# Optimization experiments

Measured on AMD Instinct MI355X. Metric: run time of the kernel, lower is better.

The kernel has to match this reference:

```python
import jax, jax.numpy as jnp
import numpy as np

D_MODEL = 1024
N_HEADS = 16
D_H = D_MODEL // N_HEADS
MAX_LEN = 2048
BATCH = 2
SEQ = 2048
EPS = 1e-8
W_SCALE = 0.02


def _rms_norm(x, w):
    # RMSNorm: x * rsqrt(mean(x^2) + eps) * w
    ms = jnp.mean(jnp.square(x), axis=-1, keepdims=True)
    return w * (x * jax.lax.rsqrt(ms + EPS))


def setup_inputs() -> dict:
    key = jax.random.key(0)
    ks = jax.random.split(key, 12)
    d = D_MODEL
    inp = {
        "x": jax.random.normal(ks[0], (BATCH, SEQ, d), dtype=jnp.float32),
        "t_bias": jnp.zeros((1,), dtype=jnp.float32),  # unused by the module
        "p_bias": jax.random.normal(ks[1], (MAX_LEN, N_HEADS), dtype=jnp.float32),
        # AMS layer params (Linear stored as [in, out])
        "wq": jax.random.normal(ks[2], (d, d), dtype=jnp.float32) * W_SCALE,
        "bq": jnp.zeros((d,), dtype=jnp.float32),
        "wk": jax.random.normal(ks[3], (d, d), dtype=jnp.float32) * W_SCALE,
        "bk": jnp.zeros((d,), dtype=jnp.float32),
        "wv": jax.random.normal(ks[4], (d, d), dtype=jnp.float32) * W_SCALE,
        "bv": jnp.zeros((d,), dtype=jnp.float32),
        "wu": jax.random.normal(ks[5], (d, d), dtype=jnp.float32) * W_SCALE,
        "bu": jnp.zeros((d,), dtype=jnp.float32),
        "g_ams": jnp.ones((d,), dtype=jnp.float32),   # shared RMSNorm weight in AMSLayer
        # MFFN layer params
        "w0": jax.random.normal(ks[6], (d, d), dtype=jnp.float32) * W_SCALE,
        "b0": jnp.zeros((d,), dtype=jnp.float32),
        "w1": jax.random.normal(ks[7], (d, 2 * d), dtype=jnp.float32) * W_SCALE,
        "b1": jnp.zeros((2 * d,), dtype=jnp.float32),
        "w2": jax.random.normal(ks[8], (d, d), dtype=jnp.float32) * W_SCALE,
        "b2": jnp.zeros((d,), dtype=jnp.float32),
        "g_mffn": jnp.ones((d,), dtype=jnp.float32),
    }
    return inp


def reference(x, t_bias, p_bias, wq, bq, wk, bk, wv, bv, wu, bu, g_ams,
              w0, b0, w1, b1, w2, b2, g_mffn):
    B, S, d = x.shape
    H, dh = N_HEADS, D_H

    # ---- AMS layer ----
    x_norm = _rms_norm(x, g_ams)

    def proj(w, b):
        # [B,S,d] -> [B,H,S,dh]
        return (x_norm @ w + b).reshape(B, S, H, dh).transpose(0, 2, 1, 3)

    q = proj(wq, bq)
    k = proj(wk, bk)
    v = proj(wv, bv)

    scale = 1.0 / np.sqrt(dh).astype(np.float32)
    score = jnp.einsum('bhsd,bhtd->bhst', q, k) * scale
    # additive positional bias: p_bias[:S].T -> [H,S], broadcast over query dim
    score = score + p_bias[:S, :].T[None, :, None, :]

    attn = jax.nn.silu(score)                        # SiLU instead of softmax
    out = jnp.einsum('bhst,bhtd->bhsd', attn, v)
    out = out.transpose(0, 2, 1, 3).reshape(B, S, d)

    u = jax.nn.silu(x_norm @ wu + bu)
    ams_out = _rms_norm(out, g_ams) * u

    # ---- MFFN layer ----
    o = (ams_out @ w0 + b0) + x
    o_norm = _rms_norm(o, g_mffn)
    x12 = o_norm @ w1 + b1
    x1, x2 = jnp.split(x12, 2, axis=-1)
    swiglu = jax.nn.silu(x1) * x2
    return (swiglu @ w2 + b2) + o
```

## Files before the change

kernel.cpp:

```cpp
#include <hip/hip_runtime.h>
#include <stdint.h>
#include <math.h>


#define D    1024
#define NH   16
#define DH   64
#define B_   2
#define S_   2048
#define ROWS 4096
#define LQ   4096
#define EPSR 1e-8f

typedef unsigned short u16;
typedef __attribute__((ext_vector_type(8))) short short8;
typedef __attribute__((ext_vector_type(4))) float f32x4;

__device__ __forceinline__ float bf2f(u16 u) {
    union { uint32_t i; float f; } c; c.i = ((uint32_t)u) << 16; return c.f;
}
__device__ __forceinline__ u16 f2bf(float f) {
    union { float f; uint32_t i; } c; c.f = f;
    uint32_t x = c.i;
    x += 0x7fffu + ((x >> 16) & 1u);
    return (u16)(x >> 16);
}
__device__ __forceinline__ uint32_t pack2bf(float a, float b) {
    union { float f; uint32_t i; } ca, cb; ca.f = a; cb.f = b;
    return __builtin_amdgcn_perm(cb.i + 0x8000u, ca.i + 0x8000u, 0x07060302);
}
#define LOG2E 1.44269504f
__device__ __forceinline__ float silu_fast(float v) {
    return v * __builtin_amdgcn_rcpf(1.0f + __builtin_amdgcn_exp2f(v * -LOG2E));
}

__global__ __launch_bounds__(256) void transpose_all_kernel(
    const float* __restrict__ wq, const float* __restrict__ wk,
    const float* __restrict__ wv, const float* __restrict__ wu,
    const float* __restrict__ w0, const float* __restrict__ w2,
    const float* __restrict__ w1,
    u16* __restrict__ wT4, u16* __restrict__ w0T,
    u16* __restrict__ w2T, u16* __restrict__ w1T)
{
    const unsigned MI = 1u << 20;
    const int z = blockIdx.z;
    const float* W; u16* WT; int N; int noff = 0;
    switch (z) {
        case 0: W = wq; WT = wT4;          N = 1024; break;
        case 1: W = wk; WT = wT4 + 1 * MI; N = 1024; break;
        case 2: W = wv; WT = wT4 + 2 * MI; N = 1024; break;
        case 3: W = wu; WT = wT4 + 3 * MI; N = 1024; break;
        case 4: W = w0; WT = w0T;          N = 1024; break;
        case 5: W = w2; WT = w2T;          N = 1024; break;
        case 6: W = w1; WT = w1T;          N = 2048; noff = 0;    break;
        default:W = w1; WT = w1T;          N = 2048; noff = 1024; break;
    }
    __shared__ float T[64][65];
    const int tid = threadIdx.x;
    const int n0 = (blockIdx.x << 6) + noff;
    const int k0 = blockIdx.y << 6;
    const int rr = tid >> 4;
    const int cc = (tid & 15) << 2;
#pragma unroll
    for (int l = 0; l < 4; ++l) {
        const int r = rr + (l << 4);
        float4 v = *(const float4*)&W[(size_t)(k0 + r) * N + n0 + cc];
        T[cc + 0][r] = v.x; T[cc + 1][r] = v.y;
        T[cc + 2][r] = v.z; T[cc + 3][r] = v.w;
    }
    __syncthreads();
    const int n  = tid >> 2;
    const int ks = (tid & 3) << 4;
#pragma unroll
    for (int m = 0; m < 4; ++m) {
        const int k = ks + (m << 2);
        float4 v = *(const float4*)&T[n][k];
        ushort4 o;
        o.x = f2bf(v.x); o.y = f2bf(v.y); o.z = f2bf(v.z); o.w = f2bf(v.w);
        *(ushort4*)&WT[(size_t)(n0 + n) * 1024 + k0 + k] = o;
    }
}

__global__ __launch_bounds__(256) void rmsnorm_kernel(
    const float* __restrict__ inf, const u16* __restrict__ inb, int ldi,
    const float* __restrict__ g,
    const u16* __restrict__ mul, int ldm,
    u16* __restrict__ out, int ldo)
{
    const int row = blockIdx.x;
    const int tid = threadIdx.x;
    const int c = tid << 2;
    float x0, x1, x2, x3;
    if (inb) {
        ushort4 xi = *(const ushort4*)&inb[(size_t)row * ldi + c];
        x0 = bf2f(xi.x); x1 = bf2f(xi.y); x2 = bf2f(xi.z); x3 = bf2f(xi.w);
    } else {
        float4 xi = *(const float4*)&inf[(size_t)row * ldi + c];
        x0 = xi.x; x1 = xi.y; x2 = xi.z; x3 = xi.w;
    }
    float ss = x0*x0 + x1*x1 + x2*x2 + x3*x3;
#pragma unroll
    for (int off = 32; off > 0; off >>= 1) ss += __shfl_down(ss, off, 64);
    __shared__ float red[4];
    if ((tid & 63) == 0) red[tid >> 6] = ss;
    __syncthreads();
    float r = rsqrtf((red[0] + red[1] + red[2] + red[3]) * (1.0f / D) + EPSR);
    float4 gv = *(const float4*)&g[c];
    float v0 = x0 * r * gv.x, v1 = x1 * r * gv.y, v2 = x2 * r * gv.z, v3 = x3 * r * gv.w;
    if (mul) {
        ushort4 mi = *(const ushort4*)&mul[(size_t)row * ldm + c];
        v0 *= bf2f(mi.x); v1 *= bf2f(mi.y); v2 *= bf2f(mi.z); v3 *= bf2f(mi.w);
    }
    ushort4 o;
    o.x = f2bf(v0); o.y = f2bf(v1); o.z = f2bf(v2); o.w = f2bf(v3);
    *(ushort4*)&out[(size_t)row * ldo + c] = o;
}

__global__ __launch_bounds__(256) void gemm128(
    const u16* __restrict__ A, const u16* __restrict__ WT,
    const float* __restrict__ bs0, const float* __restrict__ bs1,
    const float* __restrict__ bs2, const float* __restrict__ bs3,
    u16* __restrict__ outb, int ldo, int actmask,
    u16* __restrict__ VT, int vtsel)
{
    __shared__ u16 As[128 * 32];
    __shared__ u16 Bs[128 * 32];
    const int tid  = threadIdx.x;
    const int wave = tid >> 6;
    const int lane = tid & 63;
    const int lm   = lane & 15;
    const int quad = lane >> 4;
    const int row0 = blockIdx.y << 7;
    const int col0 = blockIdx.x << 7;
    const int wr = (wave >> 1) << 6;
    const int wc = (wave & 1) << 6;

    const int srow = wave * 32 + (lane >> 2);
    const int skp  = (lane & 3) << 3;
    const u16* Ag = A  + (size_t)(row0 + srow) * 1024 + skp;
    const u16* Bg = WT + (size_t)(col0 + srow) * 1024 + skp;
    u16* Asd0 = &As[(wave * 32) * 32];
    u16* Asd1 = &As[(wave * 32 + 16) * 32];
    u16* Bsd0 = &Bs[(wave * 32) * 32];
    u16* Bsd1 = &Bs[(wave * 32 + 16) * 32];

    f32x4 acc[4][4] = {};

    for (int k0 = 0; k0 < 1024; k0 += 32) {
        __syncthreads();
        __builtin_amdgcn_global_load_lds(
            (const __attribute__((address_space(1))) void*)(Ag + k0),
            (__attribute__((address_space(3))) void*)Asd0, 16, 0, 0);
        __builtin_amdgcn_global_load_lds(
            (const __attribute__((address_space(1))) void*)(Ag + 16 * 1024 + k0),
            (__attribute__((address_space(3))) void*)Asd1, 16, 0, 0);
        __builtin_amdgcn_global_load_lds(
            (const __attribute__((address_space(1))) void*)(Bg + k0),
            (__attribute__((address_space(3))) void*)Bsd0, 16, 0, 0);
        __builtin_amdgcn_global_load_lds(
            (const __attribute__((address_space(1))) void*)(Bg + 16 * 1024 + k0),
            (__attribute__((address_space(3))) void*)Bsd1, 16, 0, 0);
        __syncthreads();
        short8 af[4], bf[4];
#pragma unroll
        for (int i = 0; i < 4; ++i)
            af[i] = *(const short8*)&As[(wr + i * 16 + lm) * 32 + quad * 8];
#pragma unroll
        for (int j = 0; j < 4; ++j)
            bf[j] = *(const short8*)&Bs[(wc + j * 16 + lm) * 32 + quad * 8];
#pragma unroll
        for (int i = 0; i < 4; ++i)
#pragma unroll
            for (int j = 0; j < 4; ++j)
                acc[i][j] = __builtin_amdgcn_mfma_f32_16x16x32_bf16(af[i], bf[j], acc[i][j], 0, 0, 0);
    }
    const int sel = col0 >> 10;
    const float* bias = (sel == 0) ? bs0 : (sel == 1) ? bs1 : (sel == 2) ? bs2 : bs3;
    const int act = (actmask >> sel) & 1;
    if (VT && sel == vtsel) {
        const int b = row0 >> 11;
#pragma unroll
        for (int j = 0; j < 4; ++j) {
            const int c2 = (col0 + wc + j * 16 + lm) & 1023;
            const int h  = c2 >> 6;
            const int dh = c2 & 63;
            const float bj = bias[c2];
            u16* vrow = VT + ((size_t)(b * NH + h) * 64 + dh) * (size_t)S_;
#pragma unroll
            for (int i = 0; i < 4; ++i) {
                const int tb = (row0 & 2047) + wr + i * 16 + quad * 4;
                ushort4 o;
                o.x = f2bf(acc[i][j][0] + bj);
                o.y = f2bf(acc[i][j][1] + bj);
                o.z = f2bf(acc[i][j][2] + bj);
                o.w = f2bf(acc[i][j][3] + bj);
                *(ushort4*)&vrow[tb] = o;
            }
        }
    } else {
#pragma unroll
        for (int j = 0; j < 4; ++j) {
            const int colg = col0 + wc + j * 16 + lm;
            const float bj = bias[colg & 1023];
#pragma unroll
            for (int i = 0; i < 4; ++i) {
#pragma unroll
                for (int r = 0; r < 4; ++r) {
                    const int rowg = row0 + wr + i * 16 + quad * 4 + r;
                    float v = acc[i][j][r] + bj;
                    if (act) v = silu_fast(v);
                    outb[(size_t)rowg * ldo + colg] = f2bf(v);
                }
            }
        }
    }
}

__global__ __launch_bounds__(256) void gemm64(
    const u16* __restrict__ A, int lda, const u16* __restrict__ WT,
    const float* __restrict__ bias,
    const float* __restrict__ res,
    float* __restrict__ outf, int ldo)
{
    __shared__ u16 As[128 * 32];
    __shared__ u16 Bs[64 * 32];
    const int tid  = threadIdx.x;
    const int wave = tid >> 6;
    const int lane = tid & 63;
    const int lm   = lane & 15;
    const int quad = lane >> 4;
    const int row0 = blockIdx.y << 7;
    const int col0 = blockIdx.x << 6;
    const int wr = (wave >> 1) << 6;
    const int wc = (wave & 1) << 5;

    const int srA = wave * 32 + (lane >> 2);
    const int srB = wave * 16 + (lane >> 2);
    const int skp = (lane & 3) << 3;
    const u16* Ag = A  + (size_t)(row0 + srA) * lda + skp;
    const u16* Bg = WT + (size_t)(col0 + srB) * 1024 + skp;
    u16* Asd0 = &As[(wave * 32) * 32];
    u16* Asd1 = &As[(wave * 32 + 16) * 32];
    u16* Bsd  = &Bs[(wave * 16) * 32];

    f32x4 acc[4][2] = {};

    for (int k0 = 0; k0 < 1024; k0 += 32) {
        __syncthreads();
        __builtin_amdgcn_global_load_lds(
            (const __attribute__((address_space(1))) void*)(Ag + k0),
            (__attribute__((address_space(3))) void*)Asd0, 16, 0, 0);
        __builtin_amdgcn_global_load_lds(
            (const __attribute__((address_space(1))) void*)(Ag + (size_t)16 * lda + k0),
            (__attribute__((address_space(3))) void*)Asd1, 16, 0, 0);
        __builtin_amdgcn_global_load_lds(
            (const __attribute__((address_space(1))) void*)(Bg + k0),
            (__attribute__((address_space(3))) void*)Bsd, 16, 0, 0);
        __syncthreads();
        short8 af[4], bf[2];
#pragma unroll
        for (int i = 0; i < 4; ++i)
            af[i] = *(const short8*)&As[(wr + i * 16 + lm) * 32 + quad * 8];
#pragma unroll
        for (int j = 0; j < 2; ++j)
            bf[j] = *(const short8*)&Bs[(wc + j * 16 + lm) * 32 + quad * 8];
#pragma unroll
        for (int i = 0; i < 4; ++i)
#pragma unroll
            for (int j = 0; j < 2; ++j)
                acc[i][j] = __builtin_amdgcn_mfma_f32_16x16x32_bf16(af[i], bf[j], acc[i][j], 0, 0, 0);
    }
#pragma unroll
    for (int j = 0; j < 2; ++j) {
        const int colg = col0 + wc + j * 16 + lm;
        const float bj = bias[colg];
#pragma unroll
        for (int i = 0; i < 4; ++i) {
#pragma unroll
            for (int r = 0; r < 4; ++r) {
                const int rowg = row0 + wr + i * 16 + quad * 4 + r;
                const size_t idx = (size_t)rowg * ldo + colg;
                float v = acc[i][j][r] + bj;
                if (res) v += res[idx];
                outf[idx] = v;
            }
        }
    }
}

__global__ __launch_bounds__(256) void attn_mfma(
    const u16* __restrict__ qkvu, const u16* __restrict__ VT,
    const float* __restrict__ pb, u16* __restrict__ out)
{
    __shared__ u16 Ks[2][64 * 64];
    __shared__ u16 Vs[2][64 * 64];
    __shared__ u16 Pl[128 * 72];
    __shared__ float pbl[S_];
    const int tid  = threadIdx.x;
    const int wave = tid >> 6;
    const int lane = tid & 63;
    const int lm   = lane & 15;
    const int quad = lane >> 4;
    const int s0 = blockIdx.x << 7;
    const int h  = blockIdx.y;
    const int b  = blockIdx.z;
    const size_t base = (size_t)b * S_ * LQ + (size_t)h * DH;
    const u16* q  = qkvu + base;
    const u16* kg = qkvu + base + 1024;
    const u16* vt = VT + (size_t)(b * NH + h) * 64 * S_;
    const int sw = wave << 5;

    for (int i = tid; i < S_; i += 256) pbl[i] = pb[(size_t)i * NH + h];

    short8 qf[2][2];
#pragma unroll
    for (int ns = 0; ns < 2; ++ns)
#pragma unroll
        for (int kk = 0; kk < 2; ++kk)
            qf[ns][kk] = *(const short8*)&q[(size_t)(s0 + sw + ns * 16 + lm) * LQ + kk * 32 + quad * 8];

    const int lr  = lane >> 3;
    const int lc  = lane & 7;
    const int gch = lc ^ lr;
    const u16* kg0 = kg + (size_t)(16 * wave + lr) * LQ + gch * 8;
    const u16* vg0 = vt + (size_t)(16 * wave + lr) * S_ + gch * 8;
    const int cof0 = ((0 * 4 + quad) ^ (lm & 7)) * 8;
    const int cof1 = ((1 * 4 + quad) ^ (lm & 7)) * 8;

#define GLDS(gp, lp) __builtin_amdgcn_global_load_lds( \
        (const __attribute__((address_space(1))) void*)(gp), \
        (__attribute__((address_space(3))) void*)(lp), 16, 0, 0)

    GLDS(kg0,                     &Ks[0][(16 * wave) * 64]);
    GLDS(kg0 + (size_t)8 * LQ,    &Ks[0][(16 * wave + 8) * 64]);
    GLDS(vg0,                     &Vs[0][(16 * wave) * 64]);
    GLDS(vg0 + (size_t)8 * S_,    &Vs[0][(16 * wave + 8) * 64]);

    f32x4 accO[2][4] = {};
    __syncthreads();

    for (int t0 = 0; t0 < S_; t0 += 64) {
        const int ib = (t0 >> 6) & 1;
        const int nb = ib ^ 1;
        if (t0 + 64 < S_) {
            const size_t tn = (size_t)(t0 + 64);
            GLDS(kg0 + tn * LQ,            &Ks[nb][(16 * wave) * 64]);
            GLDS(kg0 + (tn + 8) * LQ,      &Ks[nb][(16 * wave + 8) * 64]);
            GLDS(vg0 + tn,                 &Vs[nb][(16 * wave) * 64]);
            GLDS(vg0 + tn + (size_t)8 * S_,&Vs[nb][(16 * wave + 8) * 64]);
        }
        short8 kf[4][2];
#pragma unroll
        for (int mt = 0; mt < 4; ++mt) {
            kf[mt][0] = *(const short8*)&Ks[ib][(mt * 16 + lm) * 64 + cof0];
            kf[mt][1] = *(const short8*)&Ks[ib][(mt * 16 + lm) * 64 + cof1];
        }
        f32x4 st[4][2] = {};
#pragma unroll
        for (int mt = 0; mt < 4; ++mt)
#pragma unroll
            for (int ns = 0; ns < 2; ++ns)
#pragma unroll
                for (int kk = 0; kk < 2; ++kk)
                    st[mt][ns] = __builtin_amdgcn_mfma_f32_16x16x32_bf16(kf[mt][kk], qf[ns][kk], st[mt][ns], 0, 0, 0);
#pragma unroll
        for (int mt = 0; mt < 4; ++mt) {
            const int tl = mt * 16 + quad * 4;
            float4 pbv = *(const float4*)&pbl[t0 + tl];
            const float pbr[4]  = {pbv.x, pbv.y, pbv.z, pbv.w};
            const float pbr2[4] = {pbv.x * -LOG2E, pbv.y * -LOG2E,
                                   pbv.z * -LOG2E, pbv.w * -LOG2E};
#pragma unroll
            for (int ns = 0; ns < 2; ++ns) {
                float p[4];
#pragma unroll
                for (int r = 0; r < 4; ++r) {
                    const float a = fmaf(st[mt][ns][r], 0.125f, pbr[r]);
                    const float e = __builtin_amdgcn_exp2f(
                        fmaf(st[mt][ns][r], -0.125f * LOG2E, pbr2[r]));
                    p[r] = a * __builtin_amdgcn_rcpf(1.0f + e);
                }
                uint2 pk;
                pk.x = pack2bf(p[0], p[1]);
                pk.y = pack2bf(p[2], p[3]);
                *(uint2*)&Pl[(sw + ns * 16 + lm) * 72 + tl] = pk;
            }
        }
        short8 pf[2][2], vf[4][2];
#pragma unroll
        for (int mi = 0; mi < 2; ++mi)
#pragma unroll
            for (int kk = 0; kk < 2; ++kk)
                pf[mi][kk] = *(const short8*)&Pl[(sw + mi * 16 + lm) * 72 + kk * 32 + quad * 8];
#pragma unroll
        for (int nj = 0; nj < 4; ++nj) {
            vf[nj][0] = *(const short8*)&Vs[ib][(nj * 16 + lm) * 64 + cof0];
            vf[nj][1] = *(const short8*)&Vs[ib][(nj * 16 + lm) * 64 + cof1];
        }
#pragma unroll
        for (int mi = 0; mi < 2; ++mi)
#pragma unroll
            for (int nj = 0; nj < 4; ++nj)
#pragma unroll
                for (int kk = 0; kk < 2; ++kk)
                    accO[mi][nj] = __builtin_amdgcn_mfma_f32_16x16x32_bf16(pf[mi][kk], vf[nj][kk], accO[mi][nj], 0, 0, 0);
        __syncthreads();
    }
#undef GLDS
#pragma unroll
    for (int mi = 0; mi < 2; ++mi)
#pragma unroll
        for (int nj = 0; nj < 4; ++nj)
#pragma unroll
            for (int r = 0; r < 4; ++r) {
                const int s = s0 + sw + mi * 16 + quad * 4 + r;
                out[base + (size_t)s * LQ + nj * 16 + lm] = f2bf(accO[mi][nj][r]);
            }
}

__global__ __launch_bounds__(256) void swiglu_kernel(u16* __restrict__ qkvu)
{
    const size_t e = ((size_t)blockIdx.x * 256 + threadIdx.x) << 2;
    const size_t r = e >> 10;
    const int    c = (int)(e & 1023);
    ushort4 a = *(const ushort4*)&qkvu[r * LQ + c];
    ushort4 b = *(const ushort4*)&qkvu[r * LQ + 1024 + c];
    ushort4 o;
    o.x = f2bf(silu_fast(bf2f(a.x)) * bf2f(b.x));
    o.y = f2bf(silu_fast(bf2f(a.y)) * bf2f(b.y));
    o.z = f2bf(silu_fast(bf2f(a.z)) * bf2f(b.z));
    o.w = f2bf(silu_fast(bf2f(a.w)) * bf2f(b.w));
    *(ushort4*)&qkvu[r * LQ + 2048 + c] = o;
}

extern "C" void kernel_launch(void* const* d_in, const int* in_sizes, int n_in,
                              void* d_out, int out_size, void* d_ws, size_t ws_size,
                              hipStream_t stream)
{
    const float* x      = (const float*)d_in[0];
    const float* pb     = (const float*)d_in[2];
    const float* wq     = (const float*)d_in[3];
    const float* bq     = (const float*)d_in[4];
    const float* wk     = (const float*)d_in[5];
    const float* bk     = (const float*)d_in[6];
    const float* wv     = (const float*)d_in[7];
    const float* bv     = (const float*)d_in[8];
    const float* wu     = (const float*)d_in[9];
    const float* bu     = (const float*)d_in[10];
    const float* g_ams  = (const float*)d_in[11];
    const float* w0     = (const float*)d_in[12];
    const float* b0     = (const float*)d_in[13];
    const float* w1     = (const float*)d_in[14];
    const float* b1     = (const float*)d_in[15];
    const float* w2     = (const float*)d_in[16];
    const float* b2     = (const float*)d_in[17];
    const float* g_mffn = (const float*)d_in[18];
    float* OUT = (float*)d_out;
    u16*   VT  = (u16*)d_out;

    const size_t MI = 1024 * 1024;
    u16* WS   = (u16*)d_ws;
    u16* wT4  = WS;
    u16* w0T  = WS + 4 * MI;
    u16* w2T  = WS + 5 * MI;
    u16* w1T  = WS + 6 * MI;
    u16* A0   = WS + 8 * MI;
    u16* QKVU = WS + 12 * MI;

    dim3 blk(256);

    transpose_all_kernel<<<dim3(16, 16, 8), blk, 0, stream>>>(
        wq, wk, wv, wu, w0, w2, w1, wT4, w0T, w2T, w1T);

    rmsnorm_kernel<<<ROWS, blk, 0, stream>>>(x, nullptr, D, g_ams, nullptr, 0, A0, D);
    gemm128<<<dim3(32, 32), blk, 0, stream>>>(A0, wT4, bq, bk, bv, bu,
                                              QKVU, LQ, 0b1000, VT, 2);
    attn_mfma<<<dim3(S_ / 128, NH, B_), blk, 0, stream>>>(QKVU, VT, pb, QKVU);
    rmsnorm_kernel<<<ROWS, blk, 0, stream>>>(nullptr, QKVU, LQ, g_ams, QKVU + 3072, LQ, A0, D);
    gemm64<<<dim3(16, 32), blk, 0, stream>>>(A0, D, w0T, b0, x, OUT, D);
    rmsnorm_kernel<<<ROWS, blk, 0, stream>>>(OUT, nullptr, D, g_mffn, nullptr, 0, A0, D);
    gemm128<<<dim3(16, 32), blk, 0, stream>>>(A0, w1T, b1, b1 + 1024, b1, b1,
                                              QKVU, LQ, 0, nullptr, -1);
    swiglu_kernel<<<ROWS * D / 1024, blk, 0, stream>>>(QKVU);
    gemm64<<<dim3(16, 32), blk, 0, stream>>>(QKVU + 2048, LQ, w2T, b2, OUT, OUT, D);
    (void)ws_size; (void)in_sizes; (void)n_in; (void)out_size;
}
```

Baseline: 348.9 us.

## Load attention K/V fragments directly from global memory and remap blocks for L2 locality

Removes the double-buffered LDS staging of K and V tiles (global_load_lds plus a per-iteration barrier). Each wave now loads its MFMA fragments straight from global memory, relying on L2/cache reuse across the four waves. The block index is also remapped so that consecutive blocks are spread across heads and batches, which is meant to improve L2 or XCD locality. This cuts the LDS traffic and barriers, but every wave now issues redundant global loads and the prefetch overlap that double buffering gave is lost.

```diff
diff --git a/kernel.cpp b/kernel.cpp
--- a/kernel.cpp
+++ b/kernel.cpp
@@ -292,8 +292,6 @@
     const u16* __restrict__ qkvu, const u16* __restrict__ VT,
     const float* __restrict__ pb, u16* __restrict__ out)
 {
-    __shared__ u16 Ks[2][64 * 64];
-    __shared__ u16 Vs[2][64 * 64];
     __shared__ u16 Pl[128 * 72];
     __shared__ float pbl[S_];
     const int tid  = threadIdx.x;
@@ -301,9 +299,11 @@
     const int lane = tid & 63;
     const int lm   = lane & 15;
     const int quad = lane >> 4;
-    const int s0 = blockIdx.x << 7;
-    const int h  = blockIdx.y;
-    const int b  = blockIdx.z;
+    const int flat = blockIdx.x + (blockIdx.y << 4) + (blockIdx.z << 8);
+    const int work = ((flat & 7) << 6) + (flat >> 3);
+    const int s0 = (work & 15) << 7;
+    const int h  = (work >> 4) & 15;
+    const int b  = work >> 8;
     const size_t base = (size_t)b * S_ * LQ + (size_t)h * DH;
     const u16* q  = qkvu + base;
     const u16* kg = qkvu + base + 1024;
@@ -319,41 +319,25 @@
         for (int kk = 0; kk < 2; ++kk)
             qf[ns][kk] = *(const short8*)&q[(size_t)(s0 + sw + ns * 16 + lm) * LQ + kk * 32 + quad * 8];
 
-    const int lr  = lane >> 3;
-    const int lc  = lane & 7;
-    const int gch = lc ^ lr;
-    const u16* kg0 = kg + (size_t)(16 * wave + lr) * LQ + gch * 8;
-    const u16* vg0 = vt + (size_t)(16 * wave + lr) * S_ + gch * 8;
-    const int cof0 = ((0 * 4 + quad) ^ (lm & 7)) * 8;
-    const int cof1 = ((1 * 4 + quad) ^ (lm & 7)) * 8;
-
-#define GLDS(gp, lp) __builtin_amdgcn_global_load_lds( \
-        (const __attribute__((address_space(1))) void*)(gp), \
-        (__attribute__((address_space(3))) void*)(lp), 16, 0, 0)
-
-    GLDS(kg0,                     &Ks[0][(16 * wave) * 64]);
-    GLDS(kg0 + (size_t)8 * LQ,    &Ks[0][(16 * wave + 8) * 64]);
-    GLDS(vg0,                     &Vs[0][(16 * wave) * 64]);
-    GLDS(vg0 + (size_t)8 * S_,    &Vs[0][(16 * wave + 8) * 64]);
+    const u16* kgf = kg + (size_t)lm * LQ + quad * 8;
+    const u16* vtf = vt + (size_t)lm * S_ + quad * 8;
 
     f32x4 accO[2][4] = {};
     __syncthreads();
 
+#pragma unroll 1
     for (int t0 = 0; t0 < S_; t0 += 64) {
-        const int ib = (t0 >> 6) & 1;
-        const int nb = ib ^ 1;
-        if (t0 + 64 < S_) {
-            const size_t tn = (size_t)(t0 + 64);
-            GLDS(kg0 + tn * LQ,            &Ks[nb][(16 * wave) * 64]);
-            GLDS(kg0 + (tn + 8) * LQ,      &Ks[nb][(16 * wave + 8) * 64]);
-            GLDS(vg0 + tn,                 &Vs[nb][(16 * wave) * 64]);
-            GLDS(vg0 + tn + (size_t)8 * S_,&Vs[nb][(16 * wave + 8) * 64]);
+        short8 vf[4][2];
+#pragma unroll
+        for (int nj = 0; nj < 4; ++nj) {
+            vf[nj][0] = *(const short8*)(vtf + (size_t)(nj * 16) * S_ + t0);
+            vf[nj][1] = *(const short8*)(vtf + (size_t)(nj * 16) * S_ + t0 + 32);
         }
         short8 kf[4][2];
 #pragma unroll
         for (int mt = 0; mt < 4; ++mt) {
-            kf[mt][0] = *(const short8*)&Ks[ib][(mt * 16 + lm) * 64 + cof0];
-            kf[mt][1] = *(const short8*)&Ks[ib][(mt * 16 + lm) * 64 + cof1];
+            kf[mt][0] = *(const short8*)(kgf + (size_t)(t0 + mt * 16) * LQ);
+            kf[mt][1] = *(const short8*)(kgf + (size_t)(t0 + mt * 16) * LQ + 32);
         }
         f32x4 st[4][2] = {};
 #pragma unroll
@@ -386,27 +370,20 @@
                 *(uint2*)&Pl[(sw + ns * 16 + lm) * 72 + tl] = pk;
             }
         }
-        short8 pf[2][2], vf[4][2];
+        short8 pf[2][2];
 #pragma unroll
         for (int mi = 0; mi < 2; ++mi)
 #pragma unroll
             for (int kk = 0; kk < 2; ++kk)
                 pf[mi][kk] = *(const short8*)&Pl[(sw + mi * 16 + lm) * 72 + kk * 32 + quad * 8];
 #pragma unroll
-        for (int nj = 0; nj < 4; ++nj) {
-            vf[nj][0] = *(const short8*)&Vs[ib][(nj * 16 + lm) * 64 + cof0];
-            vf[nj][1] = *(const short8*)&Vs[ib][(nj * 16 + lm) * 64 + cof1];
-        }
-#pragma unroll
         for (int mi = 0; mi < 2; ++mi)
 #pragma unroll
             for (int nj = 0; nj < 4; ++nj)
 #pragma unroll
                 for (int kk = 0; kk < 2; ++kk)
                     accO[mi][nj] = __builtin_amdgcn_mfma_f32_16x16x32_bf16(pf[mi][kk], vf[nj][kk], accO[mi][nj], 0, 0, 0);
-        __syncthreads();
-    }
-#undef GLDS
+    }
 #pragma unroll
     for (int mi = 0; mi < 2; ++mi)
 #pragma unroll
```

New measurement: 392.8 us. 1.13x slower.

## Shrink attention query tile to 64, keep P in registers via bpermute

Applied to the files above, without the earlier changes.

The attention kernel now handles 64 query rows per block (16 per wave) instead of 128. The P tile is passed from the QK accumulator layout to the PV operand layout with ds_bpermute, which removes the Pl LDS buffer and its round trip. The positional bias is pre-transposed once into a per-head contiguous buffer stored in the output scratch and read directly, and block-to-work mapping is swizzled. Occupancy is hinted at 4 blocks per CU. In exchange, the block count doubles, so each K/V tile is reloaded twice as often per query row.

```diff
diff --git a/kernel.cpp b/kernel.cpp
--- a/kernel.cpp
+++ b/kernel.cpp
@@ -81,6 +81,24 @@
     }
 }
 
+__global__ __launch_bounds__(256) void pbt_kernel(
+    const float* __restrict__ pb, float* __restrict__ pbT)
+{
+    const int tid = threadIdx.x;
+    const int r = (blockIdx.x << 7) + (tid >> 1);
+    const int c0 = (tid & 1) << 3;
+    float4 v0 = *(const float4*)&pb[(size_t)r * NH + c0];
+    float4 v1 = *(const float4*)&pb[(size_t)r * NH + c0 + 4];
+    pbT[(size_t)(c0 + 0) * S_ + r] = v0.x;
+    pbT[(size_t)(c0 + 1) * S_ + r] = v0.y;
+    pbT[(size_t)(c0 + 2) * S_ + r] = v0.z;
+    pbT[(size_t)(c0 + 3) * S_ + r] = v0.w;
+    pbT[(size_t)(c0 + 4) * S_ + r] = v1.x;
+    pbT[(size_t)(c0 + 5) * S_ + r] = v1.y;
+    pbT[(size_t)(c0 + 6) * S_ + r] = v1.z;
+    pbT[(size_t)(c0 + 7) * S_ + r] = v1.w;
+}
+
 __global__ __launch_bounds__(256) void rmsnorm_kernel(
     const float* __restrict__ inf, const u16* __restrict__ inb, int ldi,
     const float* __restrict__ g,
@@ -288,44 +306,41 @@
     }
 }
 
-__global__ __launch_bounds__(256) void attn_mfma(
+__global__ __launch_bounds__(256, 4) void attn_mfma(
     const u16* __restrict__ qkvu, const u16* __restrict__ VT,
-    const float* __restrict__ pb, u16* __restrict__ out)
+    const float* __restrict__ pbT, u16* __restrict__ out)
 {
     __shared__ u16 Ks[2][64 * 64];
     __shared__ u16 Vs[2][64 * 64];
-    __shared__ u16 Pl[128 * 72];
-    __shared__ float pbl[S_];
     const int tid  = threadIdx.x;
     const int wave = tid >> 6;
     const int lane = tid & 63;
     const int lm   = lane & 15;
     const int quad = lane >> 4;
-    const int s0 = blockIdx.x << 7;
-    const int h  = blockIdx.y;
-    const int b  = blockIdx.z;
+    const int flat = blockIdx.x + (blockIdx.y << 5) + (blockIdx.z << 9);
+    const int work = ((flat & 7) << 7) + (flat >> 3);
+    const int s0 = (work & 31) << 6;
+    const int h  = (work >> 5) & 15;
+    const int b  = work >> 9;
     const size_t base = (size_t)b * S_ * LQ + (size_t)h * DH;
     const u16* q  = qkvu + base;
     const u16* kg = qkvu + base + 1024;
     const u16* vt = VT + (size_t)(b * NH + h) * 64 * S_;
-    const int sw = wave << 5;
-
-    for (int i = tid; i < S_; i += 256) pbl[i] = pb[(size_t)i * NH + h];
-
-    short8 qf[2][2];
-#pragma unroll
-    for (int ns = 0; ns < 2; ++ns)
-#pragma unroll
-        for (int kk = 0; kk < 2; ++kk)
-            qf[ns][kk] = *(const short8*)&q[(size_t)(s0 + sw + ns * 16 + lm) * LQ + kk * 32 + quad * 8];
+    const float* pbh = pbT + (size_t)h * S_;
+
+    short8 qf[2];
+#pragma unroll
+    for (int kk = 0; kk < 2; ++kk)
+        qf[kk] = *(const short8*)&q[(size_t)(s0 + wave * 16 + lm) * LQ + kk * 32 + quad * 8];
 
     const int lr  = lane >> 3;
-    const int lc  = lane & 7;
-    const int gch = lc ^ lr;
+    const int gch = (lane & 7) ^ lr;
     const u16* kg0 = kg + (size_t)(16 * wave + lr) * LQ + gch * 8;
     const u16* vg0 = vt + (size_t)(16 * wave + lr) * S_ + gch * 8;
     const int cof0 = ((0 * 4 + quad) ^ (lm & 7)) * 8;
     const int cof1 = ((1 * 4 + quad) ^ (lm & 7)) * 8;
+    const int a0   = (lm + ((quad & 1) << 5)) << 2;
+    const bool hi  = quad >= 2;
 
 #define GLDS(gp, lp) __builtin_amdgcn_global_load_lds( \
         (const __attribute__((address_space(1))) void*)(gp), \
@@ -336,18 +351,22 @@
     GLDS(vg0,                     &Vs[0][(16 * wave) * 64]);
     GLDS(vg0 + (size_t)8 * S_,    &Vs[0][(16 * wave + 8) * 64]);
 
-    f32x4 accO[2][4] = {};
+    f32x4 accO[4] = {};
     __syncthreads();
 
     for (int t0 = 0; t0 < S_; t0 += 64) {
         const int ib = (t0 >> 6) & 1;
         const int nb = ib ^ 1;
+        float4 pbv[4];
+#pragma unroll
+        for (int mt = 0; mt < 4; ++mt)
+            pbv[mt] = *(const float4*)&pbh[t0 + mt * 16 + quad * 4];
         if (t0 + 64 < S_) {
             const size_t tn = (size_t)(t0 + 64);
-            GLDS(kg0 + tn * LQ,            &Ks[nb][(16 * wave) * 64]);
-            GLDS(kg0 + (tn + 8) * LQ,      &Ks[nb][(16 * wave + 8) * 64]);
-            GLDS(vg0 + tn,                 &Vs[nb][(16 * wave) * 64]);
-            GLDS(vg0 + tn + (size_t)8 * S_,&Vs[nb][(16 * wave + 8) * 64]);
+            GLDS(kg0 + tn * LQ,             &Ks[nb][(16 * wave) * 64]);
+            GLDS(kg0 + (tn + 8) * LQ,       &Ks[nb][(16 * wave + 8) * 64]);
+            GLDS(vg0 + tn,                  &Vs[nb][(16 * wave) * 64]);
+            GLDS(vg0 + tn + (size_t)8 * S_, &Vs[nb][(16 * wave + 8) * 64]);
         }
         short8 kf[4][2];
 #pragma unroll
@@ -355,67 +374,66 @@
             kf[mt][0] = *(const short8*)&Ks[ib][(mt * 16 + lm) * 64 + cof0];
             kf[mt][1] = *(const short8*)&Ks[ib][(mt * 16 + lm) * 64 + cof1];
         }
-        f32x4 st[4][2] = {};
+        f32x4 st[4] = {};
 #pragma unroll
         for (int mt = 0; mt < 4; ++mt)
 #pragma unroll
-            for (int ns = 0; ns < 2; ++ns)
-#pragma unroll
-                for (int kk = 0; kk < 2; ++kk)
-                    st[mt][ns] = __builtin_amdgcn_mfma_f32_16x16x32_bf16(kf[mt][kk], qf[ns][kk], st[mt][ns], 0, 0, 0);
+            for (int kk = 0; kk < 2; ++kk)
+                st[mt] = __builtin_amdgcn_mfma_f32_16x16x32_bf16(kf[mt][kk], qf[kk], st[mt], 0, 0, 0);
+        int stp[4][2];
 #pragma unroll
         for (int mt = 0; mt < 4; ++mt) {
-            const int tl = mt * 16 + quad * 4;
-            float4 pbv = *(const float4*)&pbl[t0 + tl];
-            const float pbr[4]  = {pbv.x, pbv.y, pbv.z, pbv.w};
-            const float pbr2[4] = {pbv.x * -LOG2E, pbv.y * -LOG2E,
-                                   pbv.z * -LOG2E, pbv.w * -LOG2E};
-#pragma unroll
-            for (int ns = 0; ns < 2; ++ns) {
-                float p[4];
-#pragma unroll
-                for (int r = 0; r < 4; ++r) {
-                    const float a = fmaf(st[mt][ns][r], 0.125f, pbr[r]);
-                    const float e = __builtin_amdgcn_exp2f(
-                        fmaf(st[mt][ns][r], -0.125f * LOG2E, pbr2[r]));
-                    p[r] = a * __builtin_amdgcn_rcpf(1.0f + e);
-                }
-                uint2 pk;
-                pk.x = pack2bf(p[0], p[1]);
-                pk.y = pack2bf(p[2], p[3]);
-                *(uint2*)&Pl[(sw + ns * 16 + lm) * 72 + tl] = pk;
+            const float pbr[4] = {pbv[mt].x, pbv[mt].y, pbv[mt].z, pbv[mt].w};
+            float p[4];
+#pragma unroll
+            for (int r = 0; r < 4; ++r) {
+                const float a = fmaf(st[mt][r], 0.125f, pbr[r]);
+                const float e = __builtin_amdgcn_exp2f(a * -LOG2E);
+                p[r] = a * __builtin_amdgcn_rcpf(1.0f + e);
             }
-        }
-        short8 pf[2][2], vf[4][2];
-#pragma unroll
-        for (int mi = 0; mi < 2; ++mi)
-#pragma unroll
-            for (int kk = 0; kk < 2; ++kk)
-                pf[mi][kk] = *(const short8*)&Pl[(sw + mi * 16 + lm) * 72 + kk * 32 + quad * 8];
+            stp[mt][0] = (int)pack2bf(p[0], p[1]);
+            stp[mt][1] = (int)pack2bf(p[2], p[3]);
+        }
+        short8 pf[2];
+#pragma unroll
+        for (int kk = 0; kk < 2; ++kk) {
+            const int e0 = stp[2 * kk][0],     e1 = stp[2 * kk][1];
+            const int o0 = stp[2 * kk + 1][0], o1 = stp[2 * kk + 1][1];
+            const int w0a = __builtin_amdgcn_ds_bpermute(a0,      e0);
+            const int w0b = __builtin_amdgcn_ds_bpermute(a0,      o0);
+            const int w1a = __builtin_amdgcn_ds_bpermute(a0,      e1);
+            const int w1b = __builtin_amdgcn_ds_bpermute(a0,      o1);
+            const int w2a = __builtin_amdgcn_ds_bpermute(a0 + 64, e0);
+            const int w2b = __builtin_amdgcn_ds_bpermute(a0 + 64, o0);
+            const int w3a = __builtin_amdgcn_ds_bpermute(a0 + 64, e1);
+            const int w3b = __builtin_amdgcn_ds_bpermute(a0 + 64, o1);
+            int4 pw;
+            pw.x = hi ? w0b : w0a;
+            pw.y = hi ? w1b : w1a;
+            pw.z = hi ? w2b : w2a;
+            pw.w = hi ? w3b : w3a;
+            pf[kk] = *(const short8*)&pw;
+        }
+        short8 vf[4][2];
 #pragma unroll
         for (int nj = 0; nj < 4; ++nj) {
             vf[nj][0] = *(const short8*)&Vs[ib][(nj * 16 + lm) * 64 + cof0];
             vf[nj][1] = *(const short8*)&Vs[ib][(nj * 16 + lm) * 64 + cof1];
         }
 #pragma unroll
-        for (int mi = 0; mi < 2; ++mi)
-#pragma unroll
-            for (int nj = 0; nj < 4; ++nj)
-#pragma unroll
-                for (int kk = 0; kk < 2; ++kk)
-                    accO[mi][nj] = __builtin_amdgcn_mfma_f32_16x16x32_bf16(pf[mi][kk], vf[nj][kk], accO[mi][nj], 0, 0, 0);
+        for (int nj = 0; nj < 4; ++nj)
+#pragma unroll
+            for (int kk = 0; kk < 2; ++kk)
+                accO[nj] = __builtin_amdgcn_mfma_f32_16x16x32_bf16(pf[kk], vf[nj][kk], accO[nj], 0, 0, 0);
         __syncthreads();
     }
 #undef GLDS
-#pragma unroll
-    for (int mi = 0; mi < 2; ++mi)
-#pragma unroll
-        for (int nj = 0; nj < 4; ++nj)
-#pragma unroll
-            for (int r = 0; r < 4; ++r) {
-                const int s = s0 + sw + mi * 16 + quad * 4 + r;
-                out[base + (size_t)s * LQ + nj * 16 + lm] = f2bf(accO[mi][nj][r]);
-            }
+    const int srow = s0 + wave * 16 + quad * 4;
+#pragma unroll
+    for (int nj = 0; nj < 4; ++nj)
+#pragma unroll
+        for (int r = 0; r < 4; ++r)
+            out[base + (size_t)(srow + r) * LQ + nj * 16 + lm] = f2bf(accO[nj][r]);
 }
 
 __global__ __launch_bounds__(256) void swiglu_kernel(u16* __restrict__ qkvu)
@@ -457,6 +475,7 @@
     const float* g_mffn = (const float*)d_in[18];
     float* OUT = (float*)d_out;
     u16*   VT  = (u16*)d_out;
+    float* pbT = (float*)((u16*)d_out + 4 * (1u << 20));
 
     const size_t MI = 1024 * 1024;
     u16* WS   = (u16*)d_ws;
@@ -471,11 +490,12 @@
 
     transpose_all_kernel<<<dim3(16, 16, 8), blk, 0, stream>>>(
         wq, wk, wv, wu, w0, w2, w1, wT4, w0T, w2T, w1T);
+    pbt_kernel<<<16, blk, 0, stream>>>(pb, pbT);
 
     rmsnorm_kernel<<<ROWS, blk, 0, stream>>>(x, nullptr, D, g_ams, nullptr, 0, A0, D);
     gemm128<<<dim3(32, 32), blk, 0, stream>>>(A0, wT4, bq, bk, bv, bu,
                                               QKVU, LQ, 0b1000, VT, 2);
-    attn_mfma<<<dim3(S_ / 128, NH, B_), blk, 0, stream>>>(QKVU, VT, pb, QKVU);
+    attn_mfma<<<dim3(32, 16, 2), blk, 0, stream>>>(QKVU, VT, pbT, QKVU);
     rmsnorm_kernel<<<ROWS, blk, 0, stream>>>(nullptr, QKVU, LQ, g_ams, QKVU + 3072, LQ, A0, D);
     gemm64<<<dim3(16, 32), blk, 0, stream>>>(A0, D, w0T, b0, x, OUT, D);
     rmsnorm_kernel<<<ROWS, blk, 0, stream>>>(OUT, nullptr, D, g_mffn, nullptr, 0, A0, D);
```

Measured after the change: 352.9 us. About the same (+1.2%).
